# Performance work log

Measured on AMD Instinct MI355X. Metric: run time of the kernel, lower is better.

Reference implementation:

```python
import jax, jax.numpy as jnp
import numpy as np

CH = 128
GROUPS = 8
EPS = 1e-5


def setup_inputs() -> dict:
    key = jax.random.key(0)
    ks = jax.random.split(key, 12)
    b, c, h, w = 16, CH, 64, 64
    x = jax.random.normal(ks[0], (b, c, h, w), dtype=jnp.float32)
    s = 1.0 / np.sqrt(c)
    return {
        "x": x,
        "gn_w": jnp.ones((c,), jnp.float32),
        "gn_b": jnp.zeros((c,), jnp.float32),
        "wq": jax.random.normal(ks[1], (c, c), jnp.float32) * s,
        "bq": jax.random.normal(ks[2], (c,), jnp.float32) * 0.01,
        "wk": jax.random.normal(ks[3], (c, c), jnp.float32) * s,
        "bk": jax.random.normal(ks[4], (c,), jnp.float32) * 0.01,
        "wv": jax.random.normal(ks[5], (c, c), jnp.float32) * s,
        "bv": jax.random.normal(ks[6], (c,), jnp.float32) * 0.01,
        "wf": jax.random.normal(ks[7], (c, c), jnp.float32) * s,
        "bf": jax.random.normal(ks[8], (c,), jnp.float32) * 0.01,
    }


def _group_norm(x, gamma, beta):
    b, c, h, w = x.shape
    xg = x.reshape(b, GROUPS, -1)  # [b, g, (c/g)*h*w]
    mean = xg.mean(axis=-1, keepdims=True)
    var = xg.var(axis=-1, keepdims=True)
    xn = ((xg - mean) * jax.lax.rsqrt(var + EPS)).reshape(b, c, h, w)
    return xn * gamma[None, :, None, None] + beta[None, :, None, None]


def reference(x, gn_w, gn_b, wq, bq, wk, bk, wv, bv, wf, bf):
    b, c, h, w = x.shape
    x_gn = _group_norm(x, gn_w, gn_b)
    xf = x_gn.reshape(b, c, h * w)  # [b, c, n]
    # 1x1 convs == per-position channel matmuls
    q = jnp.einsum('oc,bcn->bon', wq, xf) + bq[None, :, None]
    k = jnp.einsum('oc,bcn->bon', wk, xf) + bk[None, :, None]
    v = jnp.einsum('oc,bcn->bon', wv, xf) + bv[None, :, None]
    scale = c ** (-0.5)
    attn = jnp.einsum('bci,bcj->bij', q, k) * scale  # [b, n, n]
    attn = jax.nn.softmax(attn, axis=-1)
    # out[b,c,i] = sum_j v[b,c,j] * attn[b,i,j]
    o = jnp.einsum('bcj,bij->bci', v, attn)
    of = jnp.einsum('oc,bcn->bon', wf, o) + bf[None, :, None]
    return of.reshape(b, c, h, w) + x
```

## Files before the change

kernel.cpp:

```cpp
#include <hip/hip_runtime.h>

#define NB   16
#define NC   128
#define NPOS 4096

typedef short bf16x8 __attribute__((ext_vector_type(8)));
typedef float f32x4  __attribute__((ext_vector_type(4)));
typedef float f32x16 __attribute__((ext_vector_type(16)));
typedef unsigned int u32x4 __attribute__((ext_vector_type(4)));

#define SCF 0.12751743075095855f

static __device__ __forceinline__ unsigned short f2bf(float f) {
    unsigned int u = __builtin_bit_cast(unsigned int, f);
    u += 0x7FFFu + ((u >> 16) & 1u);
    return (unsigned short)(u >> 16);
}

static __device__ __forceinline__ unsigned int pkbf(float hi, float lo) {
    return __builtin_amdgcn_perm(__builtin_bit_cast(unsigned int, hi),
                                 __builtin_bit_cast(unsigned int, lo), 0x07060302u);
}

__global__ void wconv_kernel(const float* __restrict__ wq, const float* __restrict__ wk,
                             const float* __restrict__ wv, const float* __restrict__ wf,
                             unsigned short* __restrict__ oq, unsigned short* __restrict__ ok,
                             unsigned short* __restrict__ ov, unsigned short* __restrict__ of) {
    int i = blockIdx.x * 256 + threadIdx.x;
    oq[i] = f2bf(wq[i]); ok[i] = f2bf(wk[i]); ov[i] = f2bf(wv[i]); of[i] = f2bf(wf[i]);
}

__global__ void gnstat_kernel(const float* __restrict__ x, float* __restrict__ mean,
                              float* __restrict__ rstd) {
    int bg = blockIdx.x;
    const float* p = x + (size_t)bg * 65536;
    int t = threadIdx.x;
    float s = 0.f, q = 0.f;
    for (int it = 0; it < 64; ++it) {
        f32x4 v = *(const f32x4*)(p + it * 1024 + t * 4);
        s += v[0] + v[1] + v[2] + v[3];
        q += v[0] * v[0] + v[1] * v[1] + v[2] * v[2] + v[3] * v[3];
    }
    for (int m = 1; m < 64; m <<= 1) { s += __shfl_xor(s, m); q += __shfl_xor(q, m); }
    __shared__ float ls[4], lq[4];
    int w = t >> 6;
    if ((t & 63) == 0) { ls[w] = s; lq[w] = q; }
    __syncthreads();
    if (t == 0) {
        s = ls[0] + ls[1] + ls[2] + ls[3];
        q = lq[0] + lq[1] + lq[2] + lq[3];
        float mu  = s * (1.0f / 65536.0f);
        float var = q * (1.0f / 65536.0f) - mu * mu;
        mean[bg] = mu;
        rstd[bg] = rsqrtf(var + 1e-5f);
    }
}

__global__ __launch_bounds__(256) void qkv_kernel(
    const float* __restrict__ x, const float* __restrict__ gnw, const float* __restrict__ gnb,
    const float* __restrict__ mean, const float* __restrict__ rstd,
    const unsigned short* __restrict__ wqb, const unsigned short* __restrict__ wkb,
    const unsigned short* __restrict__ wvb,
    const float* __restrict__ bq, const float* __restrict__ bk, const float* __restrict__ bv,
    unsigned short* __restrict__ qT, unsigned short* __restrict__ Kf, unsigned short* __restrict__ Vf) {
    __shared__ __attribute__((aligned(16))) unsigned short xn[64 * 136];
    __shared__ __attribute__((aligned(16))) unsigned short bnc[64 * 128];
    const int b = blockIdx.y, i0 = blockIdx.x * 64, jt = blockIdx.x;
    const int t = threadIdx.x;
    {
        int iL = (t & 15) * 4;
        int cb = (t >> 4) * 2;
        for (int cg = 0; cg < 4; ++cg) {
            int c = cg * 32 + cb;
            int g = c >> 4;
            float mu = mean[b * 8 + g], rs = rstd[b * 8 + g];
            float ga0 = gnw[c] * rs,     be0 = gnb[c]     - mu * ga0;
            float ga1 = gnw[c + 1] * rs, be1 = gnb[c + 1] - mu * ga1;
            const float* p0 = x + ((size_t)(b * NC + c)) * NPOS + i0 + iL;
            f32x4 v0 = *(const f32x4*)p0;
            f32x4 v1 = *(const f32x4*)(p0 + NPOS);
            for (int e = 0; e < 4; ++e) {
                unsigned int u = (unsigned)f2bf(v0[e] * ga0 + be0) |
                                 ((unsigned)f2bf(v1[e] * ga1 + be1) << 16);
                *(unsigned int*)&xn[(iL + e) * 136 + c] = u;
            }
        }
    }
    __syncthreads();

    const int lane = t & 63, w = t >> 6, quad = lane >> 4, li = lane & 15;

    bf16x8 ax[4];
    for (int kc = 0; kc < 4; ++kc)
        ax[kc] = *(const bf16x8*)&xn[(w * 16 + li) * 136 + kc * 32 + quad * 8];

    for (int wt = 0; wt < 2; ++wt) {
        const unsigned short* W = wt ? wkb : wqb;
        const float* bias = wt ? bk : bq;
        const float osc = wt ? 1.0f : SCF;
        for (int nt = 0; nt < 8; ++nt) {
            f32x4 d = {0.f, 0.f, 0.f, 0.f};
            for (int kc = 0; kc < 4; ++kc) {
                bf16x8 bw = *(const bf16x8*)&W[(nt * 16 + li) * 128 + kc * 32 + quad * 8];
                d = __builtin_amdgcn_mfma_f32_16x16x32_bf16(ax[kc], bw, d, 0, 0, 0);
            }
            float bb = bias[nt * 16 + li];
            int o = nt * 16 + li;
            for (int rr = 0; rr < 4; ++rr) {
                int i = w * 16 + quad * 4 + rr;
                bnc[i * 128 + (((o >> 3) ^ (i & 7)) << 3) + (o & 7)] = f2bf((d[rr] + bb) * osc);
            }
        }
        __syncthreads();
        if (wt == 0) {
            unsigned short* dst = qT + ((size_t)b * NPOS + i0) * NC + t * 32;
            int i = t >> 2;
            for (int s = 0; s < 4; ++s) {
                int cc = (t & 3) * 4 + s;
                *(bf16x8*)(dst + s * 8) = *(const bf16x8*)&bnc[i * 128 + ((cc ^ (i & 7)) << 3)];
            }
        } else {
            unsigned short* dst = Kf + ((size_t)(b * 64 + jt)) * 8192 + t * 32;
            int F = t >> 4, jtile = F >> 3, kc = F & 7;
            for (int s = 0; s < 4; ++s) {
                int L = (t * 4 + s) & 63;
                int i = jtile * 32 + (L & 31);
                int cc = kc * 2 + (L >> 5);
                *(bf16x8*)(dst + s * 8) = *(const bf16x8*)&bnc[i * 128 + ((cc ^ (i & 7)) << 3)];
            }
        }
        __syncthreads();
    }

    bf16x8 av[2][4];
    for (int mt = 0; mt < 2; ++mt)
        for (int kc = 0; kc < 4; ++kc)
            av[mt][kc] = *(const bf16x8*)&wvb[((w * 2 + mt) * 16 + li) * 128 + kc * 32 + quad * 8];
    for (int nt = 0; nt < 4; ++nt) {
        bf16x8 bx[4];
        for (int kc = 0; kc < 4; ++kc)
            bx[kc] = *(const bf16x8*)&xn[(nt * 16 + li) * 136 + kc * 32 + quad * 8];
        for (int mt = 0; mt < 2; ++mt) {
            f32x4 d = {0.f, 0.f, 0.f, 0.f};
            for (int kc = 0; kc < 4; ++kc)
                d = __builtin_amdgcn_mfma_f32_16x16x32_bf16(av[mt][kc], bx[kc], d, 0, 0, 0);
            int o0 = (w * 2 + mt) * 16 + quad * 4;
            int j = nt * 16 + li;
            for (int rr = 0; rr < 4; ++rr) {
                int c = o0 + rr;
                bnc[c * 64 + (((j >> 3) ^ (c & 7)) << 3) + (j & 7)] = f2bf(d[rr] + bv[c]);
            }
        }
    }
    __syncthreads();
    {
        unsigned short* dst = Vf + ((size_t)(b * 64 + jt)) * 8192 + t * 32;
        int F = t >> 4, ct = F >> 2, kc2 = F & 3;
        for (int s = 0; s < 4; ++s) {
            int L = (t * 4 + s) & 63;
            int c = ct * 32 + (L & 31);
            int jc = kc2 * 2 + (L >> 5);
            *(bf16x8*)(dst + s * 8) = *(const bf16x8*)&bnc[c * 64 + ((jc ^ (c & 7)) << 3)];
        }
    }
}

static __device__ __forceinline__ void flash_iter(
    bf16x8 (&kcur)[16], bf16x8 (&knxt)[16],
    const unsigned short*& kp, const unsigned short*& vp,
    const bf16x8 (&qb)[2][8], float (&mr)[2], float (&lr)[2],
    f32x16 (&acc)[2][4], const int h) {
    bf16x8 vf[16];
    #pragma unroll
    for (int m = 0; m < 16; ++m) vf[m] = *(const bf16x8*)(vp + m * 512);
    vp += 8192;
    #pragma unroll
    for (int m = 0; m < 16; ++m) knxt[m] = *(const bf16x8*)(kp + m * 512);
    kp += 8192;

    f32x16 st[4];
    #pragma unroll
    for (int u = 0; u < 4; ++u)
        #pragma unroll
        for (int q = 0; q < 16; ++q) st[u][q] = 0.f;
    #pragma unroll
    for (int kc = 0; kc < 8; ++kc) {
        st[0] = __builtin_amdgcn_mfma_f32_32x32x16_bf16(kcur[kc],     qb[0][kc], st[0], 0, 0, 0);
        st[1] = __builtin_amdgcn_mfma_f32_32x32x16_bf16(kcur[8 + kc], qb[0][kc], st[1], 0, 0, 0);
        st[2] = __builtin_amdgcn_mfma_f32_32x32x16_bf16(kcur[kc],     qb[1][kc], st[2], 0, 0, 0);
        st[3] = __builtin_amdgcn_mfma_f32_32x32x16_bf16(kcur[8 + kc], qb[1][kc], st[3], 0, 0, 0);
    }

    #pragma unroll
    for (int ig = 0; ig < 2; ++ig) {
        float mx = st[ig * 2][0];
        #pragma unroll
        for (int q = 1; q < 16; ++q) mx = fmaxf(mx, st[ig * 2][q]);
        #pragma unroll
        for (int q = 0; q < 16; ++q) mx = fmaxf(mx, st[ig * 2 + 1][q]);
        mx = fmaxf(mx, __shfl_xor(mx, 32));
        if (__any(mx > mr[ig])) {
            float mn = fmaxf(mr[ig], mx);
            float alpha = __builtin_amdgcn_exp2f(mr[ig] - mn);
            mr[ig] = mn;
            lr[ig] *= alpha;
            #pragma unroll
            for (int ct = 0; ct < 4; ++ct)
                #pragma unroll
                for (int q = 0; q < 16; ++q) acc[ig][ct][q] *= alpha;
        }
        float mc = mr[ig] - 0.0028150156f;
        float p0[16], p1[16], rs = 0.f;
        #pragma unroll
        for (int q = 0; q < 16; ++q) {
            p0[q] = __builtin_amdgcn_exp2f(st[ig * 2][q] - mc);
            p1[q] = __builtin_amdgcn_exp2f(st[ig * 2 + 1][q] - mc);
            rs += p0[q] + p1[q];
        }
        rs += __shfl_xor(rs, 32);
        lr[ig] += rs;

        bf16x8 pfrag[4];
        #pragma unroll
        for (int hf = 0; hf < 2; ++hf) {
            const float* pp = hf ? p1 : p0;
            #pragma unroll
            for (int c2 = 0; c2 < 2; ++c2) {
                int rb = c2 * 8;
                unsigned int A0 = pkbf(pp[rb + 1], pp[rb + 0]);
                unsigned int A1 = pkbf(pp[rb + 3], pp[rb + 2]);
                unsigned int B0 = pkbf(pp[rb + 5], pp[rb + 4]);
                unsigned int B1 = pkbf(pp[rb + 7], pp[rb + 6]);
                unsigned int s0 = h ? A0 : B0, s1 = h ? A1 : B1;
                unsigned int r0 = __shfl_xor(s0, 32), r1 = __shfl_xor(s1, 32);
                u32x4 f;
                f[0] = h ? r0 : A0; f[1] = h ? r1 : A1;
                f[2] = h ? B0 : r0; f[3] = h ? B1 : r1;
                pfrag[hf * 2 + c2] = __builtin_bit_cast(bf16x8, f);
            }
        }

        #pragma unroll
        for (int ct = 0; ct < 4; ++ct)
            #pragma unroll
            for (int kc2 = 0; kc2 < 4; ++kc2)
                acc[ig][ct] = __builtin_amdgcn_mfma_f32_32x32x16_bf16(vf[ct * 4 + kc2], pfrag[kc2],
                                                                      acc[ig][ct], 0, 0, 0);
    }
}

__global__ __launch_bounds__(128, 1) void flash_kernel(
    const unsigned short* __restrict__ qT, const unsigned short* __restrict__ Kf,
    const unsigned short* __restrict__ Vf, unsigned short* __restrict__ oT) {
    const int idx = blockIdx.x;
    const int b = (idx & 7) * 2 + ((idx >> 3) & 1);
    const int r = idx >> 4;
    const int t = threadIdx.x, lane = t & 63, w = t >> 6;
    const int il = lane & 31, h = lane >> 5;
    const int iw = r * 128 + w * 64;

    bf16x8 qb[2][8];
    #pragma unroll
    for (int ig = 0; ig < 2; ++ig)
        #pragma unroll
        for (int kc = 0; kc < 8; ++kc)
            qb[ig][kc] = *(const bf16x8*)&qT[((size_t)b * NPOS + iw + ig * 32 + il) * NC + kc * 16 + h * 8];

    float mr[2] = {-1e30f, -1e30f}, lr[2] = {0.f, 0.f};
    f32x16 acc[2][4];
    #pragma unroll
    for (int ig = 0; ig < 2; ++ig)
        #pragma unroll
        for (int ct = 0; ct < 4; ++ct)
            #pragma unroll
            for (int q = 0; q < 16; ++q) acc[ig][ct][q] = 0.f;

    const unsigned short* kp = Kf + ((size_t)b * 64) * 8192 + lane * 8;
    const unsigned short* vp = Vf + ((size_t)b * 64) * 8192 + lane * 8;

    bf16x8 kA[16], kB[16];
    #pragma unroll
    for (int m = 0; m < 16; ++m) kA[m] = *(const bf16x8*)(kp + m * 512);
    kp += 8192;

    for (int jo = 0; jo < 32; ++jo) {
        flash_iter(kA, kB, kp, vp, qb, mr, lr, acc, h);
        flash_iter(kB, kA, kp, vp, qb, mr, lr, acc, h);
    }

    #pragma unroll
    for (int ig = 0; ig < 2; ++ig) {
        float inv = __builtin_amdgcn_rcpf(lr[ig]);
        unsigned short* orow = &oT[((size_t)b * NPOS + iw + ig * 32 + il) * NC];
        #pragma unroll
        for (int ct = 0; ct < 4; ++ct)
            #pragma unroll
            for (int q = 0; q < 16; q += 2) {
                int c = ct * 32 + (q & 3) + 8 * (q >> 2) + 4 * h;
                *(unsigned int*)&orow[c] = pkbf(acc[ig][ct][q + 1] * inv, acc[ig][ct][q] * inv);
            }
    }
}

__global__ __launch_bounds__(256) void proj_kernel(
    const unsigned short* __restrict__ oT, const unsigned short* __restrict__ wfb,
    const float* __restrict__ bf_, const float* __restrict__ x, float* __restrict__ out) {
    const int b = blockIdx.y, i0 = blockIdx.x * 64;
    const int t = threadIdx.x, lane = t & 63, w = t >> 6, quad = lane >> 4, li = lane & 15;
    bf16x8 aw[2][4];
    for (int mt = 0; mt < 2; ++mt)
        for (int kc = 0; kc < 4; ++kc)
            aw[mt][kc] = *(const bf16x8*)&wfb[((w * 2 + mt) * 16 + li) * 128 + kc * 32 + quad * 8];
    for (int nt = 0; nt < 4; ++nt) {
        bf16x8 bo[4];
        for (int kc = 0; kc < 4; ++kc)
            bo[kc] = *(const bf16x8*)&oT[((size_t)b * NPOS + i0 + nt * 16 + li) * NC + kc * 32 + quad * 8];
        for (int mt = 0; mt < 2; ++mt) {
            f32x4 d = {0.f, 0.f, 0.f, 0.f};
            for (int kc = 0; kc < 4; ++kc)
                d = __builtin_amdgcn_mfma_f32_16x16x32_bf16(aw[mt][kc], bo[kc], d, 0, 0, 0);
            int o0 = (w * 2 + mt) * 16 + quad * 4;
            for (int rr = 0; rr < 4; ++rr) {
                size_t idx = ((size_t)(b * NC + o0 + rr)) * NPOS + i0 + nt * 16 + li;
                out[idx] = d[rr] + bf_[o0 + rr] + x[idx];
            }
        }
    }
}

extern "C" void kernel_launch(void* const* d_in, const int* in_sizes, int n_in,
                              void* d_out, int out_size, void* d_ws, size_t ws_size,
                              hipStream_t stream) {
    const float* x   = (const float*)d_in[0];
    const float* gnw = (const float*)d_in[1];
    const float* gnb = (const float*)d_in[2];
    const float* wq  = (const float*)d_in[3];
    const float* bq  = (const float*)d_in[4];
    const float* wk  = (const float*)d_in[5];
    const float* bk  = (const float*)d_in[6];
    const float* wv  = (const float*)d_in[7];
    const float* bv  = (const float*)d_in[8];
    const float* wf  = (const float*)d_in[9];
    const float* bf_ = (const float*)d_in[10];
    float* out = (float*)d_out;

    char* ws = (char*)d_ws;
    float* mean = (float*)(ws + 0);
    float* rstd = (float*)(ws + 512);
    unsigned short* wqb = (unsigned short*)(ws + 1024);
    unsigned short* wkb = wqb + 16384;
    unsigned short* wvb = wkb + 16384;
    unsigned short* wfb = wvb + 16384;
    unsigned short* qT  = (unsigned short*)(ws + 132096);
    unsigned short* Kf  = qT + (size_t)NB * NPOS * NC;
    unsigned short* Vf  = Kf + (size_t)NB * NPOS * NC;
    unsigned short* oT  = Vf + (size_t)NB * NPOS * NC;

    wconv_kernel<<<64, 256, 0, stream>>>(wq, wk, wv, wf, wqb, wkb, wvb, wfb);
    gnstat_kernel<<<128, 256, 0, stream>>>(x, mean, rstd);
    dim3 g(64, 16);
    qkv_kernel<<<g, 256, 0, stream>>>(x, gnw, gnb, mean, rstd, wqb, wkb, wvb, bq, bk, bv, qT, Kf, Vf);
    flash_kernel<<<512, 128, 0, stream>>>(qT, Kf, Vf, oT);
    proj_kernel<<<g, 256, 0, stream>>>(oT, wfb, bf_, x, out);
}
```

Measured before the change: 343.8 us.

## Fuse output projection and residual into flash attention epilogue

The flash kernel now converts its normalized accumulators directly into bf16 MFMA B-fragments and performs the final 1x1 projection, bias add and residual add in its epilogue. This removes the separate projection kernel and the intermediate bf16 attention-output buffer round trip through global memory. The max and row-sum reductions are also rewritten as balanced trees to shorten dependency chains. The normalizer gets a small scale factor, which changes numerics slightly, and the epilogue adds register pressure and serial tail work per block.

```diff
diff --git a/kernel.cpp b/kernel.cpp
--- a/kernel.cpp
+++ b/kernel.cpp
@@ -20,6 +20,39 @@
 static __device__ __forceinline__ unsigned int pkbf(float hi, float lo) {
     return __builtin_amdgcn_perm(__builtin_bit_cast(unsigned int, hi),
                                  __builtin_bit_cast(unsigned int, lo), 0x07060302u);
+}
+
+static __device__ __forceinline__ float vmax16(const f32x16 v) {
+    float a = fmaxf(fmaxf(v[0], v[1]), fmaxf(v[2], v[3]));
+    float b = fmaxf(fmaxf(v[4], v[5]), fmaxf(v[6], v[7]));
+    float c = fmaxf(fmaxf(v[8], v[9]), fmaxf(v[10], v[11]));
+    float d = fmaxf(fmaxf(v[12], v[13]), fmaxf(v[14], v[15]));
+    return fmaxf(fmaxf(a, b), fmaxf(c, d));
+}
+
+static __device__ __forceinline__ float vsum16(const float* p) {
+    float a = (p[0] + p[1]) + (p[2] + p[3]);
+    float b = (p[4] + p[5]) + (p[6] + p[7]);
+    float c = (p[8] + p[9]) + (p[10] + p[11]);
+    float d = (p[12] + p[13]) + (p[14] + p[15]);
+    return (a + b) + (c + d);
+}
+
+static __device__ __forceinline__ void mk_bfrag_pair(const float* pp, bf16x8* dst, int h) {
+    #pragma unroll
+    for (int c2 = 0; c2 < 2; ++c2) {
+        int rb = c2 * 8;
+        unsigned int A0 = pkbf(pp[rb + 1], pp[rb + 0]);
+        unsigned int A1 = pkbf(pp[rb + 3], pp[rb + 2]);
+        unsigned int B0 = pkbf(pp[rb + 5], pp[rb + 4]);
+        unsigned int B1 = pkbf(pp[rb + 7], pp[rb + 6]);
+        unsigned int s0 = h ? A0 : B0, s1 = h ? A1 : B1;
+        unsigned int r0 = __shfl_xor(s0, 32), r1 = __shfl_xor(s1, 32);
+        u32x4 f;
+        f[0] = h ? r0 : A0; f[1] = h ? r1 : A1;
+        f[2] = h ? B0 : r0; f[3] = h ? B1 : r1;
+        dst[c2] = __builtin_bit_cast(bf16x8, f);
+    }
 }
 
 __global__ void wconv_kernel(const float* __restrict__ wq, const float* __restrict__ wk,
@@ -193,11 +226,7 @@
 
     #pragma unroll
     for (int ig = 0; ig < 2; ++ig) {
-        float mx = st[ig * 2][0];
-        #pragma unroll
-        for (int q = 1; q < 16; ++q) mx = fmaxf(mx, st[ig * 2][q]);
-        #pragma unroll
-        for (int q = 0; q < 16; ++q) mx = fmaxf(mx, st[ig * 2 + 1][q]);
+        float mx = fmaxf(vmax16(st[ig * 2]), vmax16(st[ig * 2 + 1]));
         mx = fmaxf(mx, __shfl_xor(mx, 32));
         if (__any(mx > mr[ig])) {
             float mn = fmaxf(mr[ig], mx);
@@ -210,35 +239,19 @@
                 for (int q = 0; q < 16; ++q) acc[ig][ct][q] *= alpha;
         }
         float mc = mr[ig] - 0.0028150156f;
-        float p0[16], p1[16], rs = 0.f;
+        float p0[16], p1[16];
         #pragma unroll
         for (int q = 0; q < 16; ++q) {
             p0[q] = __builtin_amdgcn_exp2f(st[ig * 2][q] - mc);
             p1[q] = __builtin_amdgcn_exp2f(st[ig * 2 + 1][q] - mc);
-            rs += p0[q] + p1[q];
-        }
+        }
+        float rs = vsum16(p0) + vsum16(p1);
         rs += __shfl_xor(rs, 32);
         lr[ig] += rs;
 
         bf16x8 pfrag[4];
-        #pragma unroll
-        for (int hf = 0; hf < 2; ++hf) {
-            const float* pp = hf ? p1 : p0;
-            #pragma unroll
-            for (int c2 = 0; c2 < 2; ++c2) {
-                int rb = c2 * 8;
-                unsigned int A0 = pkbf(pp[rb + 1], pp[rb + 0]);
-                unsigned int A1 = pkbf(pp[rb + 3], pp[rb + 2]);
-                unsigned int B0 = pkbf(pp[rb + 5], pp[rb + 4]);
-                unsigned int B1 = pkbf(pp[rb + 7], pp[rb + 6]);
-                unsigned int s0 = h ? A0 : B0, s1 = h ? A1 : B1;
-                unsigned int r0 = __shfl_xor(s0, 32), r1 = __shfl_xor(s1, 32);
-                u32x4 f;
-                f[0] = h ? r0 : A0; f[1] = h ? r1 : A1;
-                f[2] = h ? B0 : r0; f[3] = h ? B1 : r1;
-                pfrag[hf * 2 + c2] = __builtin_bit_cast(bf16x8, f);
-            }
-        }
+        mk_bfrag_pair(p0, &pfrag[0], h);
+        mk_bfrag_pair(p1, &pfrag[2], h);
 
         #pragma unroll
         for (int ct = 0; ct < 4; ++ct)
@@ -251,7 +264,8 @@
 
 __global__ __launch_bounds__(128, 1) void flash_kernel(
     const unsigned short* __restrict__ qT, const unsigned short* __restrict__ Kf,
-    const unsigned short* __restrict__ Vf, unsigned short* __restrict__ oT) {
+    const unsigned short* __restrict__ Vf, const unsigned short* __restrict__ wfb,
+    const float* __restrict__ bf_, const float* __restrict__ x, float* __restrict__ out) {
     const int idx = blockIdx.x;
     const int b = (idx & 7) * 2 + ((idx >> 3) & 1);
     const int r = idx >> 4;
@@ -288,41 +302,39 @@
         flash_iter(kB, kA, kp, vp, qb, mr, lr, acc, h);
     }
 
+    bf16x8 obf[2][8];
     #pragma unroll
     for (int ig = 0; ig < 2; ++ig) {
-        float inv = __builtin_amdgcn_rcpf(lr[ig]);
-        unsigned short* orow = &oT[((size_t)b * NPOS + iw + ig * 32 + il) * NC];
-        #pragma unroll
-        for (int ct = 0; ct < 4; ++ct)
-            #pragma unroll
-            for (int q = 0; q < 16; q += 2) {
-                int c = ct * 32 + (q & 3) + 8 * (q >> 2) + 4 * h;
-                *(unsigned int*)&orow[c] = pkbf(acc[ig][ct][q + 1] * inv, acc[ig][ct][q] * inv);
-            }
-    }
-}
-
-__global__ __launch_bounds__(256) void proj_kernel(
-    const unsigned short* __restrict__ oT, const unsigned short* __restrict__ wfb,
-    const float* __restrict__ bf_, const float* __restrict__ x, float* __restrict__ out) {
-    const int b = blockIdx.y, i0 = blockIdx.x * 64;
-    const int t = threadIdx.x, lane = t & 63, w = t >> 6, quad = lane >> 4, li = lane & 15;
-    bf16x8 aw[2][4];
-    for (int mt = 0; mt < 2; ++mt)
-        for (int kc = 0; kc < 4; ++kc)
-            aw[mt][kc] = *(const bf16x8*)&wfb[((w * 2 + mt) * 16 + li) * 128 + kc * 32 + quad * 8];
-    for (int nt = 0; nt < 4; ++nt) {
-        bf16x8 bo[4];
-        for (int kc = 0; kc < 4; ++kc)
-            bo[kc] = *(const bf16x8*)&oT[((size_t)b * NPOS + i0 + nt * 16 + li) * NC + kc * 32 + quad * 8];
-        for (int mt = 0; mt < 2; ++mt) {
-            f32x4 d = {0.f, 0.f, 0.f, 0.f};
-            for (int kc = 0; kc < 4; ++kc)
-                d = __builtin_amdgcn_mfma_f32_16x16x32_bf16(aw[mt][kc], bo[kc], d, 0, 0, 0);
-            int o0 = (w * 2 + mt) * 16 + quad * 4;
-            for (int rr = 0; rr < 4; ++rr) {
-                size_t idx = ((size_t)(b * NC + o0 + rr)) * NPOS + i0 + nt * 16 + li;
-                out[idx] = d[rr] + bf_[o0 + rr] + x[idx];
+        float inv = __builtin_amdgcn_rcpf(lr[ig]) * 1.001953125f;
+        #pragma unroll
+        for (int ct = 0; ct < 4; ++ct) {
+            float pp[16];
+            #pragma unroll
+            for (int q = 0; q < 16; ++q) pp[q] = acc[ig][ct][q] * inv;
+            mk_bfrag_pair(pp, &obf[ig][ct * 2], h);
+        }
+    }
+
+    #pragma unroll
+    for (int ot = 0; ot < 4; ++ot) {
+        bf16x8 wfA[8];
+        #pragma unroll
+        for (int kc = 0; kc < 8; ++kc)
+            wfA[kc] = *(const bf16x8*)&wfb[(ot * 32 + il) * 128 + kc * 16 + h * 8];
+        #pragma unroll
+        for (int ig = 0; ig < 2; ++ig) {
+            f32x16 d;
+            #pragma unroll
+            for (int q = 0; q < 16; ++q) d[q] = 0.f;
+            #pragma unroll
+            for (int kc = 0; kc < 8; ++kc)
+                d = __builtin_amdgcn_mfma_f32_32x32x16_bf16(wfA[kc], obf[ig][kc], d, 0, 0, 0);
+            const int ig_i = iw + ig * 32 + il;
+            #pragma unroll
+            for (int q = 0; q < 16; ++q) {
+                int o = ot * 32 + (q & 3) + 8 * (q >> 2) + 4 * h;
+                size_t a = ((size_t)(b * NC + o)) * NPOS + ig_i;
+                out[a] = d[q] + bf_[o] + x[a];
             }
         }
     }
@@ -354,12 +366,10 @@
     unsigned short* qT  = (unsigned short*)(ws + 132096);
     unsigned short* Kf  = qT + (size_t)NB * NPOS * NC;
     unsigned short* Vf  = Kf + (size_t)NB * NPOS * NC;
-    unsigned short* oT  = Vf + (size_t)NB * NPOS * NC;
 
     wconv_kernel<<<64, 256, 0, stream>>>(wq, wk, wv, wf, wqb, wkb, wvb, wfb);
     gnstat_kernel<<<128, 256, 0, stream>>>(x, mean, rstd);
     dim3 g(64, 16);
     qkv_kernel<<<g, 256, 0, stream>>>(x, gnw, gnb, mean, rstd, wqb, wkb, wvb, bq, bk, bv, qT, Kf, Vf);
-    flash_kernel<<<512, 128, 0, stream>>>(qT, Kf, Vf, oT);
-    proj_kernel<<<g, 256, 0, stream>>>(oT, wfb, bf_, x, out);
-}
+    flash_kernel<<<512, 128, 0, stream>>>(qT, Kf, Vf, wfb, bf_, x, out);
+}
```

Result: faster. 333.7 us (-2.9%).
